# Performance work log

Measured on AMD Instinct MI355X. Metric: run time of the kernel, lower is better.

The kernel has to match this reference:

```python
import jax, jax.numpy as jnp
import numpy as np

DIM = 1024
NHEAD = 16
HEAD_DIM = DIM // NHEAD
B, S, L = 1, 4096, 4096


def setup_inputs() -> dict:
    key = jax.random.key(0)
    ks = jax.random.split(key, 11)
    scale = 1.0 / np.sqrt(DIM)
    inp = {
        'query': jax.random.normal(ks[0], (B, S, DIM), dtype=jnp.float32),
        'key': jax.random.normal(ks[1], (B, L, DIM), dtype=jnp.float32),
        'value': jax.random.normal(ks[2], (B, L, DIM), dtype=jnp.float32),
        # torch nn.Linear weights: y = x @ W.T + b, W shape (out, in) = (DIM, DIM)
        'Wq': jax.random.normal(ks[3], (DIM, DIM), dtype=jnp.float32) * scale,
        'bq': jax.random.normal(ks[4], (DIM,), dtype=jnp.float32) * 0.01,
        'Wk': jax.random.normal(ks[5], (DIM, DIM), dtype=jnp.float32) * scale,
        'bk': jax.random.normal(ks[6], (DIM,), dtype=jnp.float32) * 0.01,
        'Wv': jax.random.normal(ks[7], (DIM, DIM), dtype=jnp.float32) * scale,
        'bv': jax.random.normal(ks[8], (DIM,), dtype=jnp.float32) * 0.01,
        'Wo': jax.random.normal(ks[9], (DIM, DIM), dtype=jnp.float32) * scale,
        'bo': jax.random.normal(ks[10], (DIM,), dtype=jnp.float32) * 0.01,
    }
    return inp


def _split_heads(x):
    # (B, T, D) -> (B, H, T, hd)
    b, t, _ = x.shape
    return x.reshape(b, t, NHEAD, HEAD_DIM).transpose(0, 2, 1, 3)


def reference(query, key, value, Wq, bq, Wk, bk, Wv, bv, Wo, bo):
    q = _split_heads(query @ Wq.T + bq)   # (B,H,S,hd)
    k = _split_heads(key @ Wk.T + bk)     # (B,H,L,hd)
    v = _split_heads(value @ Wv.T + bv)   # (B,H,L,hd)
    inv_sqrt_d = 1.0 / np.sqrt(HEAD_DIM).astype(np.float32)
    scores = jnp.einsum('bhsd,bhld->bhsl', q, k) * inv_sqrt_d
    probs = jax.nn.softmax(scores, axis=-1)
    ctx = jnp.einsum('bhsl,bhld->bhsd', probs, v)
    ctx = ctx.transpose(0, 2, 1, 3).reshape(query.shape[0], -1, DIM)
    return ctx @ Wo.T + bo
```

## Files before the change

kernel.cpp:

```cpp
#include <hip/hip_runtime.h>
#include <hip/hip_bf16.h>

#define DIM 1024
#define NHEAD 16
#define HD 64
#define SEQ 4096

typedef unsigned short u16;
typedef unsigned int u32;
typedef __attribute__((ext_vector_type(8))) short bf16x8;
typedef __attribute__((ext_vector_type(4))) float f32x4;
typedef __attribute__((ext_vector_type(16))) float f32x16;

__device__ __forceinline__ u16 f2bf(float x) {
  __hip_bfloat16 h = __float2bfloat16(x);
  return *reinterpret_cast<u16*>(&h);
}

__device__ __forceinline__ float bf2f(u16 u) {
  union { u32 u; float f; } c;
  c.u = ((u32)u) << 16;
  return c.f;
}

__device__ __forceinline__ float fexp2(float x) {
#if __has_builtin(__builtin_amdgcn_exp2f)
  return __builtin_amdgcn_exp2f(x);
#else
  return __expf(x * 0.69314718056f);
#endif
}

__device__ __forceinline__ u32 cvtpk(float a, float b) {
  u32 r;
  asm("v_cvt_pk_bf16_f32 %0, %1, %2" : "=v"(r) : "v"(a), "v"(b));
  return r;
}

__device__ __forceinline__ void pswap(u32& a, u32& b) {
  asm("v_permlane32_swap_b32 %0, %1" : "+v"(a), "+v"(b));
}

__device__ __forceinline__ void gload16(const u16* g, const u16* l) {
  __builtin_amdgcn_global_load_lds(
      (const __attribute__((address_space(1))) void*)g,
      (__attribute__((address_space(3))) void*)l, 16, 0, 0);
}

__device__ __forceinline__ float vsum16(const f32x16& v) {
  float a[8];
#pragma unroll
  for (int j = 0; j < 8; ++j) a[j] = v[j] + v[j + 8];
#pragma unroll
  for (int j = 0; j < 4; ++j) a[j] = a[j] + a[j + 4];
  return (a[0] + a[2]) + (a[1] + a[3]);
}

__global__ __launch_bounds__(256) void cvt_all(
    const float* __restrict__ q, const float* __restrict__ k, const float* __restrict__ v,
    const float* __restrict__ wq, const float* __restrict__ wk, const float* __restrict__ wv,
    const float* __restrict__ wo,
    u16* __restrict__ oq, u16* __restrict__ ok, u16* __restrict__ ov,
    u16* __restrict__ owq, u16* __restrict__ owk, u16* __restrict__ owv, u16* __restrict__ owo) {
  int b = blockIdx.x;
  const float* in;
  u16* out;
  int i;
  if (b < 12288) {
    int s = b >> 12;
    in = (s == 0) ? q : (s == 1) ? k : v;
    out = (s == 0) ? oq : (s == 1) ? ok : ov;
    i = (b & 4095) * 256 + threadIdx.x;
  } else {
    int bb = b - 12288;
    int s = bb >> 10;
    in = (s == 0) ? wq : (s == 1) ? wk : (s == 2) ? wv : wo;
    out = (s == 0) ? owq : (s == 1) ? owk : (s == 2) ? owv : owo;
    i = (bb & 1023) * 256 + threadIdx.x;
  }
  float4 val = ((const float4*)in)[i];
  ushort4 o;
  o.x = f2bf(val.x); o.y = f2bf(val.y); o.z = f2bf(val.z); o.w = f2bf(val.w);
  ((ushort4*)out)[i] = o;
}

__global__ __launch_bounds__(256, 3) void gemm_proj(
    const u16* __restrict__ qx, const u16* __restrict__ kx, const u16* __restrict__ vx,
    const u16* __restrict__ wqp, const u16* __restrict__ wkp, const u16* __restrict__ wvp,
    const float* __restrict__ bq, const float* __restrict__ bk, const float* __restrict__ bv,
    u16* __restrict__ Qb, u16* __restrict__ Kb, u16* __restrict__ Vt) {
  __shared__ u16 As[128][64];
  __shared__ u16 Bs[128][64];
  const int z = blockIdx.y;
  const u16 *Ag, *Bg;
  const float* bias;
  u16* outp;
  int mb, nb;
  float scale = 1.f;
  if (z == 0) {
    Ag = qx; Bg = wqp; bias = bq; outp = Qb;
    mb = blockIdx.x >> 3; nb = blockIdx.x & 7; scale = 0.18033688f;
  } else if (z == 1) {
    Ag = kx; Bg = wkp; bias = bk; outp = Kb;
    mb = blockIdx.x >> 3; nb = blockIdx.x & 7;
  } else {
    Ag = wvp; Bg = vx; bias = bv; outp = Vt;
    mb = blockIdx.x >> 5; nb = blockIdx.x & 31;
  }

  const int tid = threadIdx.x, lane = tid & 63, wid = tid >> 6;
  const int lq = lane & 15, g = lane >> 4;
  const int wr = wid >> 1, wc = wid & 1;
  const int m0 = mb * 128, n0 = nb * 128;
  const int sr = lane >> 3, ss = lane & 7;

  const u16* pA = Ag + (size_t)(m0 + wid * 32 + sr) * DIM + ((ss ^ sr) * 8);
  const u16* pB = Bg + (size_t)(n0 + wid * 32 + sr) * DIM + ((ss ^ sr) * 8);

  const f32x4 zero4 = {0.f, 0.f, 0.f, 0.f};
  f32x4 acc[4][4];
#pragma unroll
  for (int mi = 0; mi < 4; ++mi)
#pragma unroll
    for (int ni = 0; ni < 4; ++ni) acc[mi][ni] = zero4;

  for (int k0 = 0; k0 < DIM; k0 += 64) {
    __syncthreads();
#pragma unroll
    for (int i = 0; i < 4; ++i) {
      gload16(pA + i * 8 * DIM + k0, &As[wid * 32 + i * 8][0]);
      gload16(pB + i * 8 * DIM + k0, &Bs[wid * 32 + i * 8][0]);
    }
    __syncthreads();
#pragma unroll
    for (int kk = 0; kk < 2; ++kk) {
      bf16x8 a[4], b[4];
#pragma unroll
      for (int t4 = 0; t4 < 4; ++t4) {
        u32 offA = (u32)(wr * 64 + t4 * 16 + lq) * 128 + (u32)(((kk * 4 + g) ^ (lq & 7)) * 16);
        u32 offB = (u32)(wc * 64 + t4 * 16 + lq) * 128 + (u32)(((kk * 4 + g) ^ (lq & 7)) * 16);
        a[t4] = *(const bf16x8*)((const char*)As + offA);
        b[t4] = *(const bf16x8*)((const char*)Bs + offB);
      }
#pragma unroll
      for (int mi = 0; mi < 4; ++mi)
#pragma unroll
        for (int ni = 0; ni < 4; ++ni)
          acc[mi][ni] = __builtin_amdgcn_mfma_f32_16x16x32_bf16(a[mi], b[ni], acc[mi][ni], 0, 0, 0);
    }
  }

  if (z < 2) {
    float bn[4];
#pragma unroll
    for (int ni = 0; ni < 4; ++ni) bn[ni] = bias[n0 + wc * 64 + ni * 16 + lq];
#pragma unroll
    for (int mi = 0; mi < 4; ++mi)
#pragma unroll
      for (int r = 0; r < 4; ++r) {
        int mm = m0 + wr * 64 + mi * 16 + g * 4 + r;
#pragma unroll
        for (int ni = 0; ni < 4; ++ni) {
          int nn = n0 + wc * 64 + ni * 16 + lq;
          float v = (acc[mi][ni][r] + bn[ni]) * scale;
          outp[((size_t)(nn >> 6) * SEQ + mm) * 64 + (nn & 63)] = f2bf(v);
        }
      }
  } else {
#pragma unroll
    for (int mi = 0; mi < 4; ++mi)
#pragma unroll
      for (int r = 0; r < 4; ++r) {
        int mm = m0 + wr * 64 + mi * 16 + g * 4 + r;
        float bm = bias[mm];
#pragma unroll
        for (int ni = 0; ni < 4; ++ni) {
          int nn = n0 + wc * 64 + ni * 16 + lq;
          outp[(size_t)mm * SEQ + nn] = f2bf(acc[mi][ni][r] + bm);
        }
      }
  }
}

__global__ __launch_bounds__(256, 2) void gemm_out(
    const u16* __restrict__ Ag, const u16* __restrict__ Bg,
    const float* __restrict__ bias, float* __restrict__ outp) {
  __shared__ u16 As[64][64];
  __shared__ u16 Bs[128][64];
  const int tid = threadIdx.x, lane = tid & 63, wid = tid >> 6;
  const int lq = lane & 15, g = lane >> 4;
  const int wr = wid >> 1, wc = wid & 1;
  const int m0 = blockIdx.x * 64, n0 = blockIdx.y * 128;
  const int sr = lane >> 3, ss = lane & 7;

  const u16* pA = Ag + (size_t)(m0 + wid * 16 + sr) * DIM + ((ss ^ sr) * 8);
  const u16* pB = Bg + (size_t)(n0 + wid * 32 + sr) * DIM + ((ss ^ sr) * 8);

  const f32x4 zero4 = {0.f, 0.f, 0.f, 0.f};
  f32x4 acc[2][4];
#pragma unroll
  for (int mi = 0; mi < 2; ++mi)
#pragma unroll
    for (int ni = 0; ni < 4; ++ni) acc[mi][ni] = zero4;

  for (int k0 = 0; k0 < DIM; k0 += 64) {
    __syncthreads();
#pragma unroll
    for (int i = 0; i < 2; ++i)
      gload16(pA + i * 8 * DIM + k0, &As[wid * 16 + i * 8][0]);
#pragma unroll
    for (int i = 0; i < 4; ++i)
      gload16(pB + i * 8 * DIM + k0, &Bs[wid * 32 + i * 8][0]);
    __syncthreads();
#pragma unroll
    for (int kk = 0; kk < 2; ++kk) {
      bf16x8 a[2], b[4];
#pragma unroll
      for (int t4 = 0; t4 < 2; ++t4) {
        u32 offA = (u32)(wr * 32 + t4 * 16 + lq) * 128 + (u32)(((kk * 4 + g) ^ (lq & 7)) * 16);
        a[t4] = *(const bf16x8*)((const char*)As + offA);
      }
#pragma unroll
      for (int t4 = 0; t4 < 4; ++t4) {
        u32 offB = (u32)(wc * 64 + t4 * 16 + lq) * 128 + (u32)(((kk * 4 + g) ^ (lq & 7)) * 16);
        b[t4] = *(const bf16x8*)((const char*)Bs + offB);
      }
#pragma unroll
      for (int mi = 0; mi < 2; ++mi)
#pragma unroll
        for (int ni = 0; ni < 4; ++ni)
          acc[mi][ni] = __builtin_amdgcn_mfma_f32_16x16x32_bf16(a[mi], b[ni], acc[mi][ni], 0, 0, 0);
    }
  }

  float bn[4];
#pragma unroll
  for (int ni = 0; ni < 4; ++ni) bn[ni] = bias[n0 + wc * 64 + ni * 16 + lq];
#pragma unroll
  for (int mi = 0; mi < 2; ++mi)
#pragma unroll
    for (int r = 0; r < 4; ++r) {
      int mm = m0 + wr * 32 + mi * 16 + g * 4 + r;
#pragma unroll
      for (int ni = 0; ni < 4; ++ni) {
        int nn = n0 + wc * 64 + ni * 16 + lq;
        outp[(size_t)mm * DIM + nn] = acc[mi][ni][r] + bn[ni];
      }
    }
}

__global__ __launch_bounds__(256, 2) void attn32(
    const u16* __restrict__ Qb, const u16* __restrict__ Kb,
    const u16* __restrict__ Vtb, u16* __restrict__ po,
    float* __restrict__ pl) {
  __shared__ u16 Ks[2][64][64];
  __shared__ u16 Vs[2][64][64];
  const int tid = threadIdx.x, lane = tid & 63, wid = tid >> 6;
  const int q5 = lane & 31, hi = lane >> 5;
  const int bid = blockIdx.x;
  const int rest = bid >> 3;
  const int h = (bid & 7) * 2 + (rest >> 5);
  const int kv = (rest >> 4) & 1;
  const int qbase = (rest & 15) * 256 + wid * 64;

  const u16* Qg = Qb + (size_t)h * SEQ * HD;
  const u16* Kg = Kb + (size_t)h * SEQ * HD;
  const u16* Vg = Vtb + (size_t)h * HD * SEQ;

  const int sr = lane >> 3, ss = lane & 7;
  const u16* pK = Kg + (size_t)(kv * 2048 + wid * 16 + sr) * HD + ((ss ^ sr) * 8);
  const u16* pV = Vg + (size_t)(wid * 16 + sr) * SEQ + kv * 2048 + ((ss ^ sr) * 8);

  u32 roff[8];
#pragma unroll
  for (int ks = 0; ks < 4; ++ks) {
    u32 slot = (u32)((ks * 2 + hi) ^ (q5 & 7));
    roff[ks * 2] = (u32)q5 * 128 + slot * 16;
    roff[ks * 2 + 1] = (u32)(32 + q5) * 128 + slot * 16;
  }
  const char* KsB = (const char*)Ks;
  const char* VsB = (const char*)Vs;

  bf16x8 qfA[4], qfB[4];
#pragma unroll
  for (int ks = 0; ks < 4; ++ks) {
    qfA[ks] = *(const bf16x8*)(Qg + (size_t)(qbase + q5) * HD + ks * 16 + hi * 8);
    qfB[ks] = *(const bf16x8*)(Qg + (size_t)(qbase + 32 + q5) * HD + ks * 16 + hi * 8);
  }

  f32x16 oA0, oA1, oB0, oB1, zv;
#pragma unroll
  for (int j = 0; j < 16; ++j) {
    oA0[j] = 0.f; oA1[j] = 0.f; oB0[j] = 0.f; oB1[j] = 0.f; zv[j] = 0.f;
  }
  float lsumA = 0.f, lsumB = 0.f;

  gload16(pK, &Ks[0][wid * 16][0]);
  gload16(pK + 8 * HD, &Ks[0][wid * 16 + 8][0]);
  gload16(pV, &Vs[0][wid * 16][0]);
  gload16(pV + 8 * SEQ, &Vs[0][wid * 16 + 8][0]);
  const u16* pKn = pK + 64 * HD;
  const u16* pVn = pV + 64;
  __syncthreads();

  const int NT = 2048 / 64;

#define PACK_W(W, pk0, pk1)                                                   \
  _Pragma("unroll")                                                           \
  for (int kss = 0; kss < 2; ++kss) {                                         \
    {                                                                         \
      u32 a = pk0[4 * kss], b = pk0[4 * kss + 2];                             \
      u32 c = pk0[4 * kss + 1], d = pk0[4 * kss + 3];                         \
      pswap(a, b);                                                            \
      pswap(c, d);                                                            \
      union { u32 u[4]; bf16x8 v; } tt;                                       \
      tt.u[0] = a; tt.u[1] = c; tt.u[2] = b; tt.u[3] = d;                     \
      W[kss] = tt.v;                                                          \
    }                                                                         \
    {                                                                         \
      u32 a = pk1[4 * kss], b = pk1[4 * kss + 2];                             \
      u32 c = pk1[4 * kss + 1], d = pk1[4 * kss + 3];                         \
      pswap(a, b);                                                            \
      pswap(c, d);                                                            \
      union { u32 u[4]; bf16x8 v; } tt;                                       \
      tt.u[0] = a; tt.u[1] = c; tt.u[2] = b; tt.u[3] = d;                     \
      W[2 + kss] = tt.v;                                                      \
    }                                                                         \
  }

#define ATTN_BODY(CB, PF)                                                       \
  {                                                                             \
    if (PF) {                                                                   \
      gload16(pKn, &Ks[(CB) ^ 1][wid * 16][0]);                                 \
      gload16(pKn + 8 * HD, &Ks[(CB) ^ 1][wid * 16 + 8][0]);                    \
      gload16(pVn, &Vs[(CB) ^ 1][wid * 16][0]);                                 \
      gload16(pVn + 8 * SEQ, &Vs[(CB) ^ 1][wid * 16 + 8][0]);                   \
      pKn += 64 * HD;                                                           \
      pVn += 64;                                                                \
    }                                                                           \
    f32x16 sA0, sA1, sB0, sB1;                                                  \
    __builtin_amdgcn_s_setprio(1);                                              \
    {                                                                           \
      bf16x8 ka0 = *(const bf16x8*)(KsB + (CB) * 8192 + roff[0]);               \
      bf16x8 ka1 = *(const bf16x8*)(KsB + (CB) * 8192 + roff[1]);               \
      sA0 = __builtin_amdgcn_mfma_f32_32x32x16_bf16(ka0, qfA[0], zv, 0, 0, 0);  \
      sA1 = __builtin_amdgcn_mfma_f32_32x32x16_bf16(ka1, qfA[0], zv, 0, 0, 0);  \
      sB0 = __builtin_amdgcn_mfma_f32_32x32x16_bf16(ka0, qfB[0], zv, 0, 0, 0);  \
      sB1 = __builtin_amdgcn_mfma_f32_32x32x16_bf16(ka1, qfB[0], zv, 0, 0, 0);  \
    }                                                                           \
    _Pragma("unroll")                                                           \
    for (int ks = 1; ks < 4; ++ks) {                                            \
      bf16x8 ka0 = *(const bf16x8*)(KsB + (CB) * 8192 + roff[ks * 2]);          \
      bf16x8 ka1 = *(const bf16x8*)(KsB + (CB) * 8192 + roff[ks * 2 + 1]);      \
      sA0 = __builtin_amdgcn_mfma_f32_32x32x16_bf16(ka0, qfA[ks], sA0, 0, 0, 0);\
      sA1 = __builtin_amdgcn_mfma_f32_32x32x16_bf16(ka1, qfA[ks], sA1, 0, 0, 0);\
      sB0 = __builtin_amdgcn_mfma_f32_32x32x16_bf16(ka0, qfB[ks], sB0, 0, 0, 0);\
      sB1 = __builtin_amdgcn_mfma_f32_32x32x16_bf16(ka1, qfB[ks], sB1, 0, 0, 0);\
    }                                                                           \
    __builtin_amdgcn_s_setprio(0);                                              \
    _Pragma("unroll")                                                           \
    for (int j = 0; j < 16; ++j) sA0[j] = fexp2(sA0[j]);                        \
    _Pragma("unroll")                                                           \
    for (int j = 0; j < 16; ++j) sA1[j] = fexp2(sA1[j]);                        \
    _Pragma("unroll")                                                           \
    for (int j = 0; j < 16; ++j) sB0[j] = fexp2(sB0[j]);                        \
    _Pragma("unroll")                                                           \
    for (int j = 0; j < 16; ++j) sB1[j] = fexp2(sB1[j]);                        \
    lsumA += vsum16(sA0) + vsum16(sA1);                                         \
    lsumB += vsum16(sB0) + vsum16(sB1);                                         \
    u32 pkA0[8], pkA1[8], pkB0[8], pkB1[8];                                     \
    _Pragma("unroll")                                                           \
    for (int i2 = 0; i2 < 8; ++i2) {                                            \
      pkA0[i2] = cvtpk(sA0[2 * i2], sA0[2 * i2 + 1]);                           \
      pkA1[i2] = cvtpk(sA1[2 * i2], sA1[2 * i2 + 1]);                           \
      pkB0[i2] = cvtpk(sB0[2 * i2], sB0[2 * i2 + 1]);                           \
      pkB1[i2] = cvtpk(sB1[2 * i2], sB1[2 * i2 + 1]);                           \
    }                                                                           \
    bf16x8 WA[4], WB[4];                                                        \
    PACK_W(WA, pkA0, pkA1)                                                      \
    PACK_W(WB, pkB0, pkB1)                                                      \
    __builtin_amdgcn_s_setprio(1);                                              \
    _Pragma("unroll")                                                           \
    for (int ks = 0; ks < 4; ++ks) {                                            \
      bf16x8 va0 = *(const bf16x8*)(VsB + (CB) * 8192 + roff[ks * 2]);          \
      bf16x8 va1 = *(const bf16x8*)(VsB + (CB) * 8192 + roff[ks * 2 + 1]);      \
      oA0 = __builtin_amdgcn_mfma_f32_32x32x16_bf16(va0, WA[ks], oA0, 0, 0, 0); \
      oA1 = __builtin_amdgcn_mfma_f32_32x32x16_bf16(va1, WA[ks], oA1, 0, 0, 0); \
      oB0 = __builtin_amdgcn_mfma_f32_32x32x16_bf16(va0, WB[ks], oB0, 0, 0, 0); \
      oB1 = __builtin_amdgcn_mfma_f32_32x32x16_bf16(va1, WB[ks], oB1, 0, 0, 0); \
    }                                                                           \
    __builtin_amdgcn_s_setprio(0);                                              \
    __syncthreads();                                                            \
  }

  for (int t = 0; t < NT; t += 2) {
    ATTN_BODY(0, true);
    ATTN_BODY(1, (t + 2 < NT));
  }
#undef ATTN_BODY
#undef PACK_W

  lsumA += __shfl_xor(lsumA, 32);
  lsumB += __shfl_xor(lsumB, 32);
  float invA = 1.f / lsumA;
  float invB = 1.f / lsumB;
  size_t ridxA = (size_t)(kv * 16 + h) * 4096 + qbase + q5;
  size_t ridxB = ridxA + 32;
  u16* cpA = po + ridxA * 64;
  u16* cpB = po + ridxB * 64;
#pragma unroll
  for (int rg = 0; rg < 4; ++rg) {
    ushort4 pa, pb;
    pa.x = f2bf(oA0[rg * 4 + 0] * invA); pa.y = f2bf(oA0[rg * 4 + 1] * invA);
    pa.z = f2bf(oA0[rg * 4 + 2] * invA); pa.w = f2bf(oA0[rg * 4 + 3] * invA);
    pb.x = f2bf(oA1[rg * 4 + 0] * invA); pb.y = f2bf(oA1[rg * 4 + 1] * invA);
    pb.z = f2bf(oA1[rg * 4 + 2] * invA); pb.w = f2bf(oA1[rg * 4 + 3] * invA);
    *(ushort4*)(cpA + rg * 8 + 4 * hi) = pa;
    *(ushort4*)(cpA + 32 + rg * 8 + 4 * hi) = pb;
    pa.x = f2bf(oB0[rg * 4 + 0] * invB); pa.y = f2bf(oB0[rg * 4 + 1] * invB);
    pa.z = f2bf(oB0[rg * 4 + 2] * invB); pa.w = f2bf(oB0[rg * 4 + 3] * invB);
    pb.x = f2bf(oB1[rg * 4 + 0] * invB); pb.y = f2bf(oB1[rg * 4 + 1] * invB);
    pb.z = f2bf(oB1[rg * 4 + 2] * invB); pb.w = f2bf(oB1[rg * 4 + 3] * invB);
    *(ushort4*)(cpB + rg * 8 + 4 * hi) = pa;
    *(ushort4*)(cpB + 32 + rg * 8 + 4 * hi) = pb;
  }
  if (hi == 0) {
    pl[ridxA] = lsumA;
    pl[ridxB] = lsumB;
  }
}

__global__ __launch_bounds__(256) void combine(
    const u16* __restrict__ po, const float* __restrict__ pl,
    u16* __restrict__ cx) {
  const int tid = threadIdx.x;
  const int R = blockIdx.x * 64 + (tid >> 2);
  const int h = R >> 12, q = R & 4095;
  const int dbase = (tid & 3) * 16;
  const int idx0 = R;
  const int idx1 = R + 16 * 4096;
  float l0 = pl[idx0], l1 = pl[idx1];
  float inv = 1.f / (l0 + l1);
  float a0 = l0 * inv, a1 = l1 * inv;
  const u16* p0 = po + (size_t)idx0 * 64 + dbase;
  const u16* p1 = po + (size_t)idx1 * 64 + dbase;
  u16* cp = cx + (size_t)q * DIM + h * 64 + dbase;
#pragma unroll
  for (int v = 0; v < 2; ++v) {
    bf16x8 x0 = *(const bf16x8*)(p0 + v * 8);
    bf16x8 x1 = *(const bf16x8*)(p1 + v * 8);
    union { u16 u[8]; bf16x8 v8; } r;
#pragma unroll
    for (int j = 0; j < 8; ++j)
      r.u[j] = f2bf(a0 * bf2f((u16)x0[j]) + a1 * bf2f((u16)x1[j]));
    *(bf16x8*)(cp + v * 8) = r.v8;
  }
}

extern "C" void kernel_launch(void* const* d_in, const int* in_sizes, int n_in,
                              void* d_out, int out_size, void* d_ws, size_t ws_size,
                              hipStream_t stream) {
  const float* query = (const float*)d_in[0];
  const float* key_  = (const float*)d_in[1];
  const float* value = (const float*)d_in[2];
  const float* Wq = (const float*)d_in[3]; const float* bq = (const float*)d_in[4];
  const float* Wk = (const float*)d_in[5]; const float* bk = (const float*)d_in[6];
  const float* Wv = (const float*)d_in[7]; const float* bv = (const float*)d_in[8];
  const float* Wo = (const float*)d_in[9]; const float* bo = (const float*)d_in[10];

  char* ws = (char*)d_ws;
  const size_t MB = 1024 * 1024;
  u16* qx = (u16*)(ws);
  u16* kx = (u16*)(ws + 8 * MB);
  u16* vx = (u16*)(ws + 16 * MB);
  u16* wq = (u16*)(ws + 24 * MB);
  u16* wk = (u16*)(ws + 26 * MB);
  u16* wv = (u16*)(ws + 28 * MB);
  u16* wo = (u16*)(ws + 30 * MB);
  u16* Qb = (u16*)(ws + 32 * MB);
  u16* Kb = (u16*)(ws + 40 * MB);
  u16* Vt = (u16*)(ws + 48 * MB);
  u16* cx = (u16*)(ws + 56 * MB);
  u16* po = (u16*)(ws);
  float* pl = (float*)(ws + 16 * MB);

  cvt_all<<<dim3(16384), 256, 0, stream>>>(query, key_, value, Wq, Wk, Wv, Wo,
                                           qx, kx, vx, wq, wk, wv, wo);

  gemm_proj<<<dim3(256, 3), 256, 0, stream>>>(qx, kx, vx, wq, wk, wv,
                                              bq, bk, bv, Qb, Kb, Vt);

  attn32<<<dim3(512), 256, 0, stream>>>(Qb, Kb, Vt, po, pl);

  combine<<<dim3(1024), 256, 0, stream>>>(po, pl, cx);

  gemm_out<<<dim3(64, 8), 256, 0, stream>>>(cx, wo, bo, (float*)d_out);
}
```

Measured before the change: 153.9 us.

## Fuse activation fp32->bf16 conversion into projection GEMM and split-KV combine into output GEMM

The activation conversion pass is removed: the projection GEMM now reads fp32 query/key/value directly, converts to bf16 in registers, and writes swizzled tiles into LDS. Only the weights are still pre-converted. The separate combine kernel is also removed, with the output GEMM merging the two split-KV partial outputs using their softmax sums while staging its A tile. This avoids writing and re-reading bf16 copies of the activations and the context, and drops two launches. In exchange, the GEMM prologues load synchronously through registers instead of async global-to-LDS loads, and each output-GEMM N-block repeats the combine work.

```diff
diff --git a/kernel.cpp b/kernel.cpp
--- a/kernel.cpp
+++ b/kernel.cpp
@@ -56,28 +56,16 @@
   return (a[0] + a[2]) + (a[1] + a[3]);
 }
 
-__global__ __launch_bounds__(256) void cvt_all(
-    const float* __restrict__ q, const float* __restrict__ k, const float* __restrict__ v,
-    const float* __restrict__ wq, const float* __restrict__ wk, const float* __restrict__ wv,
-    const float* __restrict__ wo,
-    u16* __restrict__ oq, u16* __restrict__ ok, u16* __restrict__ ov,
-    u16* __restrict__ owq, u16* __restrict__ owk, u16* __restrict__ owv, u16* __restrict__ owo) {
+__global__ __launch_bounds__(256) void cvt_w(
+    const float* __restrict__ wq, const float* __restrict__ wk,
+    const float* __restrict__ wv, const float* __restrict__ wo,
+    u16* __restrict__ owq, u16* __restrict__ owk,
+    u16* __restrict__ owv, u16* __restrict__ owo) {
   int b = blockIdx.x;
-  const float* in;
-  u16* out;
-  int i;
-  if (b < 12288) {
-    int s = b >> 12;
-    in = (s == 0) ? q : (s == 1) ? k : v;
-    out = (s == 0) ? oq : (s == 1) ? ok : ov;
-    i = (b & 4095) * 256 + threadIdx.x;
-  } else {
-    int bb = b - 12288;
-    int s = bb >> 10;
-    in = (s == 0) ? wq : (s == 1) ? wk : (s == 2) ? wv : wo;
-    out = (s == 0) ? owq : (s == 1) ? owk : (s == 2) ? owv : owo;
-    i = (bb & 1023) * 256 + threadIdx.x;
-  }
+  int s = b >> 10;
+  const float* in = (s == 0) ? wq : (s == 1) ? wk : (s == 2) ? wv : wo;
+  u16* out = (s == 0) ? owq : (s == 1) ? owk : (s == 2) ? owv : owo;
+  int i = (b & 1023) * 256 + threadIdx.x;
   float4 val = ((const float4*)in)[i];
   ushort4 o;
   o.x = f2bf(val.x); o.y = f2bf(val.y); o.z = f2bf(val.z); o.w = f2bf(val.w);
@@ -85,26 +73,27 @@
 }
 
 __global__ __launch_bounds__(256, 3) void gemm_proj(
-    const u16* __restrict__ qx, const u16* __restrict__ kx, const u16* __restrict__ vx,
+    const float* __restrict__ qf, const float* __restrict__ kf, const float* __restrict__ vf,
     const u16* __restrict__ wqp, const u16* __restrict__ wkp, const u16* __restrict__ wvp,
     const float* __restrict__ bq, const float* __restrict__ bk, const float* __restrict__ bv,
     u16* __restrict__ Qb, u16* __restrict__ Kb, u16* __restrict__ Vt) {
   __shared__ u16 As[128][64];
   __shared__ u16 Bs[128][64];
   const int z = blockIdx.y;
-  const u16 *Ag, *Bg;
+  const float* actf;
+  const u16* Wg;
   const float* bias;
   u16* outp;
   int mb, nb;
   float scale = 1.f;
   if (z == 0) {
-    Ag = qx; Bg = wqp; bias = bq; outp = Qb;
+    actf = qf; Wg = wqp; bias = bq; outp = Qb;
     mb = blockIdx.x >> 3; nb = blockIdx.x & 7; scale = 0.18033688f;
   } else if (z == 1) {
-    Ag = kx; Bg = wkp; bias = bk; outp = Kb;
+    actf = kf; Wg = wkp; bias = bk; outp = Kb;
     mb = blockIdx.x >> 3; nb = blockIdx.x & 7;
   } else {
-    Ag = wvp; Bg = vx; bias = bv; outp = Vt;
+    actf = vf; Wg = wvp; bias = bv; outp = Vt;
     mb = blockIdx.x >> 5; nb = blockIdx.x & 31;
   }
 
@@ -114,8 +103,12 @@
   const int m0 = mb * 128, n0 = nb * 128;
   const int sr = lane >> 3, ss = lane & 7;
 
-  const u16* pA = Ag + (size_t)(m0 + wid * 32 + sr) * DIM + ((ss ^ sr) * 8);
-  const u16* pB = Bg + (size_t)(n0 + wid * 32 + sr) * DIM + ((ss ^ sr) * 8);
+  const int act0 = (z < 2) ? m0 : n0;
+  const int w0 = (z < 2) ? n0 : m0;
+  u16 (*XS)[64] = (z < 2) ? As : Bs;
+  u16 (*WS)[64] = (z < 2) ? Bs : As;
+
+  const u16* pW = Wg + (size_t)(w0 + wid * 32 + sr) * DIM + ((ss ^ sr) * 8);
 
   const f32x4 zero4 = {0.f, 0.f, 0.f, 0.f};
   f32x4 acc[4][4];
@@ -127,9 +120,18 @@
   for (int k0 = 0; k0 < DIM; k0 += 64) {
     __syncthreads();
 #pragma unroll
-    for (int i = 0; i < 4; ++i) {
-      gload16(pA + i * 8 * DIM + k0, &As[wid * 32 + i * 8][0]);
-      gload16(pB + i * 8 * DIM + k0, &Bs[wid * 32 + i * 8][0]);
+    for (int i = 0; i < 4; ++i)
+      gload16(pW + i * 8 * DIM + k0, &WS[wid * 32 + i * 8][0]);
+#pragma unroll
+    for (int p = 0; p < 4; ++p) {
+      int rl = wid * 32 + p * 8 + sr;
+      const float* src = actf + (size_t)(act0 + rl) * DIM + k0 + ss * 8;
+      float4 fa = ((const float4*)src)[0];
+      float4 fb = ((const float4*)src)[1];
+      union { u32 u[4]; bf16x8 v; } t;
+      t.u[0] = cvtpk(fa.x, fa.y); t.u[1] = cvtpk(fa.z, fa.w);
+      t.u[2] = cvtpk(fb.x, fb.y); t.u[3] = cvtpk(fb.z, fb.w);
+      *(bf16x8*)&XS[rl][(ss ^ sr) * 8] = t.v;
     }
     __syncthreads();
 #pragma unroll
@@ -183,8 +185,9 @@
 }
 
 __global__ __launch_bounds__(256, 2) void gemm_out(
-    const u16* __restrict__ Ag, const u16* __restrict__ Bg,
-    const float* __restrict__ bias, float* __restrict__ outp) {
+    const u16* __restrict__ po, const float* __restrict__ pl,
+    const u16* __restrict__ Bg, const float* __restrict__ bias,
+    float* __restrict__ outp) {
   __shared__ u16 As[64][64];
   __shared__ u16 Bs[128][64];
   const int tid = threadIdx.x, lane = tid & 63, wid = tid >> 6;
@@ -193,8 +196,8 @@
   const int m0 = blockIdx.x * 64, n0 = blockIdx.y * 128;
   const int sr = lane >> 3, ss = lane & 7;
 
-  const u16* pA = Ag + (size_t)(m0 + wid * 16 + sr) * DIM + ((ss ^ sr) * 8);
   const u16* pB = Bg + (size_t)(n0 + wid * 32 + sr) * DIM + ((ss ^ sr) * 8);
+  const size_t PO_STRIDE = (size_t)16 * 4096 * 64;
 
   const f32x4 zero4 = {0.f, 0.f, 0.f, 0.f};
   f32x4 acc[2][4];
@@ -204,13 +207,32 @@
     for (int ni = 0; ni < 4; ++ni) acc[mi][ni] = zero4;
 
   for (int k0 = 0; k0 < DIM; k0 += 64) {
+    const int hh = k0 >> 6;
     __syncthreads();
-#pragma unroll
-    for (int i = 0; i < 2; ++i)
-      gload16(pA + i * 8 * DIM + k0, &As[wid * 16 + i * 8][0]);
 #pragma unroll
     for (int i = 0; i < 4; ++i)
       gload16(pB + i * 8 * DIM + k0, &Bs[wid * 32 + i * 8][0]);
+#pragma unroll
+    for (int p = 0; p < 2; ++p) {
+      int rl = wid * 16 + p * 8 + sr;
+      int s = m0 + rl;
+      int ridx = hh * 4096 + s;
+      float l0 = pl[ridx], l1 = pl[ridx + 16 * 4096];
+      float inv = 1.f / (l0 + l1);
+      float a0 = l0 * inv, a1 = l1 * inv;
+      const u16* p0 = po + (size_t)ridx * 64 + ss * 8;
+      const u16* p1 = p0 + PO_STRIDE;
+      bf16x8 x0 = *(const bf16x8*)p0;
+      bf16x8 x1 = *(const bf16x8*)p1;
+      float f[8];
+#pragma unroll
+      for (int j = 0; j < 8; ++j)
+        f[j] = a0 * bf2f((u16)x0[j]) + a1 * bf2f((u16)x1[j]);
+      union { u32 u[4]; bf16x8 v; } t;
+      t.u[0] = cvtpk(f[0], f[1]); t.u[1] = cvtpk(f[2], f[3]);
+      t.u[2] = cvtpk(f[4], f[5]); t.u[3] = cvtpk(f[6], f[7]);
+      *(bf16x8*)&As[rl][(ss ^ sr) * 8] = t.v;
+    }
     __syncthreads();
 #pragma unroll
     for (int kk = 0; kk < 2; ++kk) {
@@ -430,33 +452,6 @@
   }
 }
 
-__global__ __launch_bounds__(256) void combine(
-    const u16* __restrict__ po, const float* __restrict__ pl,
-    u16* __restrict__ cx) {
-  const int tid = threadIdx.x;
-  const int R = blockIdx.x * 64 + (tid >> 2);
-  const int h = R >> 12, q = R & 4095;
-  const int dbase = (tid & 3) * 16;
-  const int idx0 = R;
-  const int idx1 = R + 16 * 4096;
-  float l0 = pl[idx0], l1 = pl[idx1];
-  float inv = 1.f / (l0 + l1);
-  float a0 = l0 * inv, a1 = l1 * inv;
-  const u16* p0 = po + (size_t)idx0 * 64 + dbase;
-  const u16* p1 = po + (size_t)idx1 * 64 + dbase;
-  u16* cp = cx + (size_t)q * DIM + h * 64 + dbase;
-#pragma unroll
-  for (int v = 0; v < 2; ++v) {
-    bf16x8 x0 = *(const bf16x8*)(p0 + v * 8);
-    bf16x8 x1 = *(const bf16x8*)(p1 + v * 8);
-    union { u16 u[8]; bf16x8 v8; } r;
-#pragma unroll
-    for (int j = 0; j < 8; ++j)
-      r.u[j] = f2bf(a0 * bf2f((u16)x0[j]) + a1 * bf2f((u16)x1[j]));
-    *(bf16x8*)(cp + v * 8) = r.v8;
-  }
-}
-
 extern "C" void kernel_launch(void* const* d_in, const int* in_sizes, int n_in,
                               void* d_out, int out_size, void* d_ws, size_t ws_size,
                               hipStream_t stream) {
@@ -470,9 +465,6 @@
 
   char* ws = (char*)d_ws;
   const size_t MB = 1024 * 1024;
-  u16* qx = (u16*)(ws);
-  u16* kx = (u16*)(ws + 8 * MB);
-  u16* vx = (u16*)(ws + 16 * MB);
   u16* wq = (u16*)(ws + 24 * MB);
   u16* wk = (u16*)(ws + 26 * MB);
   u16* wv = (u16*)(ws + 28 * MB);
@@ -480,19 +472,15 @@
   u16* Qb = (u16*)(ws + 32 * MB);
   u16* Kb = (u16*)(ws + 40 * MB);
   u16* Vt = (u16*)(ws + 48 * MB);
-  u16* cx = (u16*)(ws + 56 * MB);
   u16* po = (u16*)(ws);
   float* pl = (float*)(ws + 16 * MB);
 
-  cvt_all<<<dim3(16384), 256, 0, stream>>>(query, key_, value, Wq, Wk, Wv, Wo,
-                                           qx, kx, vx, wq, wk, wv, wo);
-
-  gemm_proj<<<dim3(256, 3), 256, 0, stream>>>(qx, kx, vx, wq, wk, wv,
+  cvt_w<<<dim3(4096), 256, 0, stream>>>(Wq, Wk, Wv, Wo, wq, wk, wv, wo);
+
+  gemm_proj<<<dim3(256, 3), 256, 0, stream>>>(query, key_, value, wq, wk, wv,
                                               bq, bk, bv, Qb, Kb, Vt);
 
   attn32<<<dim3(512), 256, 0, stream>>>(Qb, Kb, Vt, po, pl);
 
-  combine<<<dim3(1024), 256, 0, stream>>>(po, pl, cx);
-
-  gemm_out<<<dim3(64, 8), 256, 0, stream>>>(cx, wo, bo, (float*)d_out);
-}
+  gemm_out<<<dim3(64, 8), 256, 0, stream>>>(po, pl, wo, bo, (float*)d_out);
+}
```

New measurement: 177.2 us. 15.1% more time.
